# Performance work log

Measured on AMD Instinct MI355X. Metric: run time of the kernel, lower is better.

The kernel has to match this reference:

```python
import jax, jax.numpy as jnp
import numpy as np

NEG_FILL = -1.0e9
PROB_MIN = 1e-9


def _lstm_cell(x, h, c, w_ih, w_hh, b_ih, b_hh):
    # PyTorch gate order: input, forget, cell(g), output
    gates = x @ w_ih.T + h @ w_hh.T + b_ih + b_hh
    i, f, g, o = jnp.split(gates, 4, axis=-1)
    c_new = jax.nn.sigmoid(f) * c + jax.nn.sigmoid(i) * jnp.tanh(g)
    h_new = jax.nn.sigmoid(o) * jnp.tanh(c_new)
    return h_new, c_new


def setup_inputs() -> dict:
    key = jax.random.key(0)
    B, T, D, H, W = 2048, 100, 128, 256, 256
    ks = jax.random.split(key, 16)
    s_d = 1.0 / np.sqrt(D)
    s_h = 1.0 / np.sqrt(H)
    s_w = 1.0 / np.sqrt(W)
    return {
        "targets": jax.random.normal(ks[0], (B, T, D), jnp.float32),
        "h0": jax.random.normal(ks[1], (1, B, H), jnp.float32),
        "c0": jax.random.normal(ks[2], (1, B, H), jnp.float32),
        "enc_w_ih": jax.random.normal(ks[3], (4 * H, D), jnp.float32) * s_d,
        "enc_w_hh": jax.random.normal(ks[4], (4 * H, H), jnp.float32) * s_h,
        "enc_b_ih": jax.random.normal(ks[5], (4 * H,), jnp.float32) * s_h,
        "enc_b_hh": jax.random.normal(ks[6], (4 * H,), jnp.float32) * s_h,
        "dec_w_ih": jax.random.normal(ks[7], (4 * H, D), jnp.float32) * s_d,
        "dec_w_hh": jax.random.normal(ks[8], (4 * H, H), jnp.float32) * s_h,
        "dec_b_ih": jax.random.normal(ks[9], (4 * H,), jnp.float32) * s_h,
        "dec_b_hh": jax.random.normal(ks[10], (4 * H,), jnp.float32) * s_h,
        "W1": jax.random.normal(ks[11], (W, H), jnp.float32) * s_h,
        "W2": jax.random.normal(ks[12], (W, H), jnp.float32) * s_h,
        "vt": jax.random.normal(ks[13], (W,), jnp.float32) * s_w,
    }


def reference(targets, h0, c0, enc_w_ih, enc_w_hh, enc_b_ih, enc_b_hh,
              dec_w_ih, dec_w_hh, dec_b_ih, dec_b_hh, W1, W2, vt):
    B, T, D = targets.shape
    H = enc_w_hh.shape[1]

    # ---- encoder LSTM (batch_first, zero initial state) ----
    def enc_step(carry, x_t):
        h, c = carry
        h, c = _lstm_cell(x_t, h, c, enc_w_ih, enc_w_hh, enc_b_ih, enc_b_hh)
        return (h, c), h

    z = jnp.zeros((B, H), targets.dtype)
    _, enc_h = jax.lax.scan(enc_step, (z, z), jnp.swapaxes(targets, 0, 1))
    encoder_states = jnp.swapaxes(enc_h, 0, 1)  # [B, T, H]

    blend1 = encoder_states @ W1.T  # [B, T, W]

    a1 = jnp.arange(B)
    init = (h0[0], c0[0], jnp.zeros((B, T), dtype=bool), jnp.zeros_like(targets[:, 0]))

    def dec_step(carry, _):
        h, c, selected, dec_in = carry
        h, c = _lstm_cell(dec_in, h, c, dec_w_ih, dec_w_hh, dec_b_ih, dec_b_hh)
        blend2 = h @ W2.T                                   # [B, W]
        scores = jnp.tanh(blend1 + blend2[:, None, :]) @ vt  # [B, T]
        scores = jnp.where(selected, NEG_FILL, scores)
        sel = jnp.argmax(scores, axis=-1)                    # [B]
        selected = selected.at[a1, sel].set(True)
        probs = jnp.maximum(jax.nn.softmax(scores, axis=-1), PROB_MIN)
        dec_in = targets[a1, sel]                            # [B, D]
        return (h, c, selected, dec_in), probs

    _, probs = jax.lax.scan(dec_step, init, None, length=T)
    return jnp.swapaxes(probs, 0, 1)  # [B, T, T]
```

## Files before the change

### kernel.cpp

```cpp
#include <hip/hip_runtime.h>
#include <math.h>
#include <stdint.h>

#define BB   2048
#define TT   100
#define DD   128
#define HH   256
#define NEGF -1.0e9f

typedef __attribute__((ext_vector_type(8))) short short8_t;
typedef __attribute__((ext_vector_type(4))) float f32x4;

#define MFMA16(a,b,c) __builtin_amdgcn_mfma_f32_16x16x32_bf16((a),(b),(c),0,0,0)

__device__ __forceinline__ float sigmoidf_(float x){ return 1.0f/(1.0f+expf(-x)); }

__device__ __forceinline__ float tanh_fast(float x){
  x = fminf(15.f, fmaxf(-15.f, x));
  const float e = __expf(x + x);
  return (e - 1.f) * __builtin_amdgcn_rcpf(e + 1.f);
}

__device__ __forceinline__ void bf16_split3(float x, unsigned short &h,
                                            unsigned short &m, unsigned short &l){
  const unsigned u = __float_as_uint(x);
  const unsigned r = u + 0x7FFFu + ((u >> 16) & 1u);
  h = (unsigned short)(r >> 16);
  const float rem = x - __uint_as_float(r & 0xFFFF0000u);
  const unsigned u2 = __float_as_uint(rem);
  const unsigned r2 = u2 + 0x7FFFu + ((u2 >> 16) & 1u);
  m = (unsigned short)(r2 >> 16);
  const float rem2 = rem - __uint_as_float(r2 & 0xFFFF0000u);
  l = (unsigned short)(__float_as_uint(rem2) >> 16);
}

__global__ __launch_bounds__(256) void k_split3(const float* __restrict__ src,
    unsigned short* __restrict__ hi, unsigned short* __restrict__ mi,
    unsigned short* __restrict__ lo, int n){
  const int i = blockIdx.x*256 + threadIdx.x;
  if(i < n){ unsigned short h,m,l; bf16_split3(src[i], h, m, l);
             hi[i]=h; mi[i]=m; lo[i]=l; }
}

__global__ __launch_bounds__(256) void k_zero_i32(int* __restrict__ p, int n){
  int i = blockIdx.x*256 + threadIdx.x;
  if(i < n) p[i] = 0;
}

#define MFMA_X6(aH,aM,aL,bH,bM,bL,acc)            \
  do{ acc = MFMA16(aM, bM, acc);                  \
      acc = MFMA16(aH, bL, acc);                  \
      acc = MFMA16(aL, bH, acc);                  \
      acc = MFMA16(aH, bM, acc);                  \
      acc = MFMA16(aM, bH, acc);                  \
      acc = MFMA16(aH, bH, acc); }while(0)

__global__ __launch_bounds__(128) void k_gates_cell(
    const float* __restrict__ Xp, int ldx,
    const float* __restrict__ Hp,
    const unsigned short* __restrict__ WihH, const unsigned short* __restrict__ WihM,
    const unsigned short* __restrict__ WihL,
    const unsigned short* __restrict__ WhhH, const unsigned short* __restrict__ WhhM,
    const unsigned short* __restrict__ WhhL,
    const float* __restrict__ bih, const float* __restrict__ bhh,
    const float* __restrict__ Cp,
    float* __restrict__ Hout, float* __restrict__ Cout,
    float* __restrict__ Hcopy, int hstride)
{
  __shared__ alignas(16) unsigned short AsH[64*40], AsM[64*40], AsL[64*40];
  __shared__ alignas(16) unsigned short WsH[64*40], WsM[64*40], WsL[64*40];
  const int tid  = threadIdx.x;
  const int lane = tid & 63;
  const int wv   = tid >> 6;
  const int l15  = lane & 15;
  const int l4   = lane >> 4;
  const int j0   = blockIdx.x * 16;
  const int m0   = blockIdx.y * 64;

  f32x4 acc[2][4];
  #pragma unroll
  for(int a=0;a<2;a++)
    #pragma unroll
    for(int s=0;s<4;s++)
      #pragma unroll
      for(int e=0;e<4;e++) acc[a][s][e] = 0.f;

  for(int phase=0; phase<2; phase++){
    const float* Am; int lda;
    const unsigned short *WH, *WM, *WL; int ldw, nt;
    if(phase==0){ if(!Xp) continue; Am=Xp; lda=ldx;
                  WH=WihH; WM=WihM; WL=WihL; ldw=DD; nt=4; }
    else        { if(!Hp) continue; Am=Hp; lda=HH;
                  WH=WhhH; WM=WhhM; WL=WhhL; ldw=HH; nt=8; }
    for(int kt=0; kt<nt; kt++){
      const int k0 = kt*32;
      __syncthreads();
      #pragma unroll
      for(int it=0; it<4; it++){
        const int q  = it*128 + tid;
        const int r  = q >> 3;
        const int kq = (q & 7) << 2;
        const float4 v = *(const float4*)(Am + (size_t)(m0+r)*lda + k0 + kq);
        unsigned short h0,m0_,l0,h1,m1_,l1,h2,m2_,l2,h3,m3_,l3;
        bf16_split3(v.x,h0,m0_,l0); bf16_split3(v.y,h1,m1_,l1);
        bf16_split3(v.z,h2,m2_,l2); bf16_split3(v.w,h3,m3_,l3);
        *(ushort4*)&AsH[r*40+kq] = make_ushort4(h0,h1,h2,h3);
        *(ushort4*)&AsM[r*40+kq] = make_ushort4(m0_,m1_,m2_,m3_);
        *(ushort4*)&AsL[r*40+kq] = make_ushort4(l0,l1,l2,l3);
      }
      #pragma unroll
      for(int half=0; half<3; half++){
        const unsigned short* __restrict__ Wg = (half==0)?WH:((half==1)?WM:WL);
        unsigned short* Ws = (half==0)?WsH:((half==1)?WsM:WsL);
        #pragma unroll
        for(int it=0; it<2; it++){
          const int q  = it*128 + tid;
          const int c  = q >> 2;
          const int kq = (q & 3) << 3;
          const int n  = ((c>>4)*HH) + j0 + (c & 15);
          *(uint4*)&Ws[c*40+kq] = *(const uint4*)(Wg + (size_t)n*ldw + k0 + kq);
        }
      }
      __syncthreads();
      short8_t aH[2], aM[2], aL[2];
      #pragma unroll
      for(int fm=0; fm<2; fm++){
        const int r = wv*32 + fm*16 + l15;
        aH[fm] = *(const short8_t*)&AsH[r*40 + l4*8];
        aM[fm] = *(const short8_t*)&AsM[r*40 + l4*8];
        aL[fm] = *(const short8_t*)&AsL[r*40 + l4*8];
      }
      #pragma unroll
      for(int s=0; s<4; s++){
        const int c = s*16 + l15;
        const short8_t bH = *(const short8_t*)&WsH[c*40 + l4*8];
        const short8_t bM = *(const short8_t*)&WsM[c*40 + l4*8];
        const short8_t bL = *(const short8_t*)&WsL[c*40 + l4*8];
        #pragma unroll
        for(int fm=0; fm<2; fm++){
          MFMA_X6(aH[fm],aM[fm],aL[fm], bH,bM,bL, acc[fm][s]);
        }
      }
    }
  }

  const int j = j0 + l15;
  const float bi0 = bih[       j] + bhh[       j];
  const float bf0 = bih[  HH + j] + bhh[  HH + j];
  const float bg0 = bih[2*HH + j] + bhh[2*HH + j];
  const float bo0 = bih[3*HH + j] + bhh[3*HH + j];
  #pragma unroll
  for(int fm=0; fm<2; fm++){
    #pragma unroll
    for(int r=0; r<4; r++){
      const int m = m0 + wv*32 + fm*16 + l4*4 + r;
      const size_t idx = (size_t)m*HH + j;
      const float iv = acc[fm][0][r] + bi0;
      const float fv = acc[fm][1][r] + bf0;
      const float gv = acc[fm][2][r] + bg0;
      const float ov = acc[fm][3][r] + bo0;
      const float cp = Cp ? Cp[idx] : 0.f;
      const float cn = sigmoidf_(fv)*cp + sigmoidf_(iv)*tanhf(gv);
      const float hn = sigmoidf_(ov)*tanhf(cn);
      Cout[idx] = cn;
      Hout[idx] = hn;
      if(Hcopy) Hcopy[(size_t)m*hstride + j] = hn;
    }
  }
}

__global__ __launch_bounds__(128) void k_blend2(
    const float* __restrict__ Hin,
    const unsigned short* __restrict__ W2H, const unsigned short* __restrict__ W2M,
    const unsigned short* __restrict__ W2L,
    float* __restrict__ out)
{
  __shared__ alignas(16) unsigned short AsH[32*40], AsM[32*40], AsL[32*40];
  __shared__ alignas(16) unsigned short WsH[64*40], WsM[64*40], WsL[64*40];
  const int tid  = threadIdx.x;
  const int lane = tid & 63;
  const int wv   = tid >> 6;
  const int l15  = lane & 15;
  const int l4   = lane >> 4;
  const int n0   = blockIdx.x * 64;
  const int m0   = blockIdx.y * 32;

  f32x4 acc[4];
  #pragma unroll
  for(int s=0;s<4;s++)
    #pragma unroll
    for(int e=0;e<4;e++) acc[s][e] = 0.f;

  for(int kt=0; kt<8; kt++){
    const int k0 = kt*32;
    __syncthreads();
    #pragma unroll
    for(int it=0; it<2; it++){
      const int q  = it*128 + tid;
      const int r  = q >> 3;
      const int kq = (q & 7) << 2;
      const float4 v = *(const float4*)(Hin + (size_t)(m0+r)*HH + k0 + kq);
      unsigned short h0,m0_,l0,h1,m1_,l1,h2,m2_,l2,h3,m3_,l3;
      bf16_split3(v.x,h0,m0_,l0); bf16_split3(v.y,h1,m1_,l1);
      bf16_split3(v.z,h2,m2_,l2); bf16_split3(v.w,h3,m3_,l3);
      *(ushort4*)&AsH[r*40+kq] = make_ushort4(h0,h1,h2,h3);
      *(ushort4*)&AsM[r*40+kq] = make_ushort4(m0_,m1_,m2_,m3_);
      *(ushort4*)&AsL[r*40+kq] = make_ushort4(l0,l1,l2,l3);
    }
    #pragma unroll
    for(int half=0; half<3; half++){
      const unsigned short* __restrict__ Wg = (half==0)?W2H:((half==1)?W2M:W2L);
      unsigned short* Ws = (half==0)?WsH:((half==1)?WsM:WsL);
      #pragma unroll
      for(int it=0; it<2; it++){
        const int q  = it*128 + tid;
        const int c  = q >> 2;
        const int kq = (q & 3) << 3;
        const int n  = n0 + c;
        *(uint4*)&Ws[c*40+kq] = *(const uint4*)(Wg + (size_t)n*HH + k0 + kq);
      }
    }
    __syncthreads();
    const int r = wv*16 + l15;
    const short8_t aH = *(const short8_t*)&AsH[r*40 + l4*8];
    const short8_t aM = *(const short8_t*)&AsM[r*40 + l4*8];
    const short8_t aL = *(const short8_t*)&AsL[r*40 + l4*8];
    #pragma unroll
    for(int s=0; s<4; s++){
      const int c = s*16 + l15;
      const short8_t bH = *(const short8_t*)&WsH[c*40 + l4*8];
      const short8_t bM = *(const short8_t*)&WsM[c*40 + l4*8];
      const short8_t bL = *(const short8_t*)&WsL[c*40 + l4*8];
      MFMA_X6(aH,aM,aL, bH,bM,bL, acc[s]);
    }
  }
  #pragma unroll
  for(int s=0; s<4; s++)
    #pragma unroll
    for(int r=0; r<4; r++)
      out[(size_t)(m0 + wv*16 + l4*4 + r)*HH + n0 + s*16 + l15] = acc[s][r];
}

__global__ __launch_bounds__(128) void k_blend1(
    float* __restrict__ blend1,
    const unsigned short* __restrict__ W1H, const unsigned short* __restrict__ W1M,
    const unsigned short* __restrict__ W1L)
{
  __shared__ alignas(16) unsigned short AsH[32*264], AsM[32*264], AsL[32*264];
  const int tid  = threadIdx.x;
  const int lane = tid & 63;
  const int wv   = tid >> 6;
  const int l15  = lane & 15;
  const int l4   = lane >> 4;
  const size_t r0 = (size_t)blockIdx.x * 32;

  #pragma unroll
  for(int it=0; it<16; it++){
    const int q  = it*128 + tid;
    const int r  = q >> 6;
    const int kq = (q & 63) << 2;
    const float4 v = *(const float4*)(blend1 + (r0+r)*256 + kq);
    unsigned short h0,m0_,l0,h1,m1_,l1,h2,m2_,l2,h3,m3_,l3;
    bf16_split3(v.x,h0,m0_,l0); bf16_split3(v.y,h1,m1_,l1);
    bf16_split3(v.z,h2,m2_,l2); bf16_split3(v.w,h3,m3_,l3);
    *(ushort4*)&AsH[r*264+kq] = make_ushort4(h0,h1,h2,h3);
    *(ushort4*)&AsM[r*264+kq] = make_ushort4(m0_,m1_,m2_,m3_);
    *(ushort4*)&AsL[r*264+kq] = make_ushort4(l0,l1,l2,l3);
  }
  __syncthreads();

  f32x4 acc[16];
  #pragma unroll
  for(int s=0;s<16;s++)
    #pragma unroll
    for(int e=0;e<4;e++) acc[s][e] = 0.f;

  const int rb = wv*16;
  for(int kt=0; kt<8; kt++){
    const int k0 = kt*32;
    const short8_t aH = *(const short8_t*)&AsH[(rb+l15)*264 + k0 + l4*8];
    const short8_t aM = *(const short8_t*)&AsM[(rb+l15)*264 + k0 + l4*8];
    const short8_t aL = *(const short8_t*)&AsL[(rb+l15)*264 + k0 + l4*8];
    #pragma unroll
    for(int fn=0; fn<16; fn++){
      const int n = fn*16 + l15;
      const short8_t bH = *(const short8_t*)(W1H + (size_t)n*256 + k0 + l4*8);
      const short8_t bM = *(const short8_t*)(W1M + (size_t)n*256 + k0 + l4*8);
      const short8_t bL = *(const short8_t*)(W1L + (size_t)n*256 + k0 + l4*8);
      MFMA_X6(aH,aM,aL, bH,bM,bL, acc[fn]);
    }
  }
  #pragma unroll
  for(int fn=0; fn<16; fn++)
    #pragma unroll
    for(int r=0; r<4; r++)
      blend1[(r0 + rb + l4*4 + r)*256 + fn*16 + l15] = acc[fn][r];
}

__global__ __launch_bounds__(256) void k_scores(
    const float* __restrict__ blend1,
    const float* __restrict__ blend2,
    const float* __restrict__ vt,
    const float* __restrict__ targets,
    int*  __restrict__ selected,
    float* __restrict__ dec_in,
    float* __restrict__ out,
    int s)
{
  __shared__ float vt_s[256], b2_s[256], sc[128];
  __shared__ float M_s, S_s;
  __shared__ int sel_s;
  const int b = blockIdx.x;
  const int tid = threadIdx.x;
  const int lane = tid & 63;
  const int wave = tid >> 6;

  vt_s[tid] = vt[tid];
  b2_s[tid] = blend2[(size_t)b*256 + tid];
  __syncthreads();

  const float4 bb = *(const float4*)&b2_s[lane*4];
  const float4 vv = *(const float4*)&vt_s[lane*4];

  for(int it=0; it<25; it++){
    const int t = wave + it*4;
    const float4 x = *(const float4*)(blend1 + ((size_t)b*TT + t)*256 + lane*4);
    float p;
    p = tanh_fast(x.x + bb.x) * vv.x;
    p = fmaf(tanh_fast(x.y + bb.y), vv.y, p);
    p = fmaf(tanh_fast(x.z + bb.z), vv.z, p);
    p = fmaf(tanh_fast(x.w + bb.w), vv.w, p);
    #pragma unroll
    for(int off=32; off>=1; off>>=1) p += __shfl_xor(p, off, 64);
    if(lane == 0) sc[t] = p;
  }
  __syncthreads();

  if(wave == 0){
    float m1 = selected[(size_t)b*TT + lane] ? NEGF : sc[lane];
    sc[lane] = m1;
    float bestv = m1; int besti = lane;
    float m2 = 0.f;
    const int t2 = lane + 64;
    if(t2 < TT){
      m2 = selected[(size_t)b*TT + t2] ? NEGF : sc[t2];
      sc[t2] = m2;
      if(m2 > bestv){ bestv = m2; besti = t2; }
    }
    #pragma unroll
    for(int off=32; off>=1; off>>=1){
      const float ov = __shfl_xor(bestv, off, 64);
      const int   oi = __shfl_xor(besti, off, 64);
      if(ov > bestv || (ov == bestv && oi < besti)){ bestv = ov; besti = oi; }
    }
    float e = __expf(m1 - bestv);
    if(t2 < TT) e += __expf(m2 - bestv);
    #pragma unroll
    for(int off=32; off>=1; off>>=1) e += __shfl_xor(e, off, 64);
    if(lane == 0){
      M_s = bestv; S_s = e; sel_s = besti;
      selected[(size_t)b*TT + besti] = 1;
    }
  }
  __syncthreads();

  const int sel = sel_s;
  if(tid < TT){
    float p = __expf(sc[tid] - M_s) / S_s;
    out[(size_t)b*TT*TT + (size_t)s*TT + tid] = fmaxf(p, 1e-9f);
  }
  if(tid < DD){
    dec_in[(size_t)b*DD + tid] = targets[((size_t)b*TT + sel)*DD + tid];
  }
}

extern "C" void kernel_launch(void* const* d_in, const int* in_sizes, int n_in,
                              void* d_out, int out_size, void* d_ws, size_t ws_size,
                              hipStream_t stream)
{
  (void)in_sizes; (void)n_in; (void)out_size; (void)ws_size;
  const float* targets  = (const float*)d_in[0];
  const float* h0       = (const float*)d_in[1];
  const float* c0       = (const float*)d_in[2];
  const float* enc_w_ih = (const float*)d_in[3];
  const float* enc_w_hh = (const float*)d_in[4];
  const float* enc_b_ih = (const float*)d_in[5];
  const float* enc_b_hh = (const float*)d_in[6];
  const float* dec_w_ih = (const float*)d_in[7];
  const float* dec_w_hh = (const float*)d_in[8];
  const float* dec_b_ih = (const float*)d_in[9];
  const float* dec_b_hh = (const float*)d_in[10];
  const float* W1       = (const float*)d_in[11];
  const float* W2       = (const float*)d_in[12];
  const float* vt       = (const float*)d_in[13];
  float* out = (float*)d_out;

  float* ws      = (float*)d_ws;
  float* blend1  = ws;
  float* hA      = blend1 + (size_t)BB*TT*256;
  float* hB      = hA + (size_t)BB*HH;
  float* cA      = hB + (size_t)BB*HH;
  float* cB      = cA + (size_t)BB*HH;
  float* blend2  = cB + (size_t)BB*HH;
  float* dec_in  = blend2 + (size_t)BB*HH;
  int*   selected= (int*)(dec_in + (size_t)BB*DD);

  char* pc = (char*)(selected + (size_t)BB*TT);
  pc = (char*)(((uintptr_t)pc + 63) & ~(uintptr_t)63);
  unsigned short* q = (unsigned short*)pc;
  unsigned short* ewihH = q; q += (size_t)1024*128;
  unsigned short* ewihM = q; q += (size_t)1024*128;
  unsigned short* ewihL = q; q += (size_t)1024*128;
  unsigned short* ewhhH = q; q += (size_t)1024*256;
  unsigned short* ewhhM = q; q += (size_t)1024*256;
  unsigned short* ewhhL = q; q += (size_t)1024*256;
  unsigned short* dwihH = q; q += (size_t)1024*128;
  unsigned short* dwihM = q; q += (size_t)1024*128;
  unsigned short* dwihL = q; q += (size_t)1024*128;
  unsigned short* dwhhH = q; q += (size_t)1024*256;
  unsigned short* dwhhM = q; q += (size_t)1024*256;
  unsigned short* dwhhL = q; q += (size_t)1024*256;
  unsigned short* w1H   = q; q += (size_t)256*256;
  unsigned short* w1M   = q; q += (size_t)256*256;
  unsigned short* w1L   = q; q += (size_t)256*256;
  unsigned short* w2H   = q; q += (size_t)256*256;
  unsigned short* w2M   = q; q += (size_t)256*256;
  unsigned short* w2L   = q; q += (size_t)256*256;

  k_split3<<<(1024*128+255)/256, 256, 0, stream>>>(enc_w_ih, ewihH, ewihM, ewihL, 1024*128);
  k_split3<<<(1024*256+255)/256, 256, 0, stream>>>(enc_w_hh, ewhhH, ewhhM, ewhhL, 1024*256);
  k_split3<<<(1024*128+255)/256, 256, 0, stream>>>(dec_w_ih, dwihH, dwihM, dwihL, 1024*128);
  k_split3<<<(1024*256+255)/256, 256, 0, stream>>>(dec_w_hh, dwhhH, dwhhM, dwhhL, 1024*256);
  k_split3<<<(256*256+255)/256,  256, 0, stream>>>(W1, w1H, w1M, w1L, 256*256);
  k_split3<<<(256*256+255)/256,  256, 0, stream>>>(W2, w2H, w2M, w2L, 256*256);

  k_zero_i32<<<(BB*TT + 255)/256, 256, 0, stream>>>(selected, BB*TT);

  for(int t=0; t<TT; t++){
    const float* Hp = (t==0) ? nullptr : ((t&1) ? hA : hB);
    const float* Cp = (t==0) ? nullptr : ((t&1) ? cA : cB);
    float* Ho = (t&1) ? hB : hA;
    float* Co = (t&1) ? cB : cA;
    k_gates_cell<<<dim3(16,32), 128, 0, stream>>>(
        targets + (size_t)t*DD, TT*DD,
        Hp, ewihH, ewihM, ewihL, ewhhH, ewhhM, ewhhL, enc_b_ih, enc_b_hh, Cp,
        Ho, Co, blend1 + (size_t)t*256, TT*256);
  }

  k_blend1<<<BB*TT/32, 128, 0, stream>>>(blend1, w1H, w1M, w1L);

  for(int s=0; s<TT; s++){
    const float* Hp = (s==0) ? h0 : ((s&1) ? hA : hB);
    const float* Cp = (s==0) ? c0 : ((s&1) ? cA : cB);
    float* Ho = (s&1) ? hB : hA;
    float* Co = (s&1) ? cB : cA;
    const float* Xp = (s==0) ? nullptr : dec_in;
    k_gates_cell<<<dim3(16,32), 128, 0, stream>>>(
        Xp, DD, Hp, dwihH, dwihM, dwihL, dwhhH, dwhhM, dwhhL, dec_b_ih, dec_b_hh, Cp,
        Ho, Co, nullptr, 0);
    k_blend2<<<dim3(4,64), 128, 0, stream>>>(Ho, w2H, w2M, w2L, blend2);
    k_scores<<<BB, 256, 0, stream>>>(blend1, blend2, vt, targets, selected,
                                     dec_in, out, s);
  }
}
```

Measured before the change: 14.68 ms.

## Fuse encoder and decoder recurrences into persistent per-batch-slice kernels

Replaces the roughly 400 per-timestep launches (gates, blend2, scores) with two persistent kernels. Each kernel owns 16 batch rows across all timesteps and keeps h, c and selection state in registers and LDS. Weights are prepacked into an MFMA-fragment layout with the input and hidden parts concatenated into one K=384 GEMM, and blend2 becomes an fp32 FMA loop over a transposed W2. Only 128 blocks run, so each block streams the full packed weight set from global or L2 on every step, and occupancy is low.

Measured after the change: 15.94 ms. +8.6%, slower.

```diff
diff --git a/kernel.cpp b/kernel.cpp
--- a/kernel.cpp
+++ b/kernel.cpp
@@ -2,16 +2,30 @@
 #include <math.h>
 #include <stdint.h>
 
-#define BB   2048
-#define TT   100
-#define DD   128
-#define HH   256
+#define BB 2048
+#define TT 100
+#define DD 128
+#define HH 256
 #define NEGF -1.0e9f
+
+#define NBLK 128
+#define ROWS 16
+#define NTHR 512
+#define KTOT 384
+#define NKF  12
+#define ASTR 392
 
 typedef __attribute__((ext_vector_type(8))) short short8_t;
 typedef __attribute__((ext_vector_type(4))) float f32x4;
 
 #define MFMA16(a,b,c) __builtin_amdgcn_mfma_f32_16x16x32_bf16((a),(b),(c),0,0,0)
+#define MFMA_X6(aH,aM,aL,bH,bM,bL,acc)            \
+  do{ acc = MFMA16(aM, bM, acc);                  \
+      acc = MFMA16(aH, bL, acc);                  \
+      acc = MFMA16(aL, bH, acc);                  \
+      acc = MFMA16(aH, bM, acc);                  \
+      acc = MFMA16(aM, bH, acc);                  \
+      acc = MFMA16(aH, bH, acc); }while(0)
 
 __device__ __forceinline__ float sigmoidf_(float x){ return 1.0f/(1.0f+expf(-x)); }
 
@@ -42,203 +56,317 @@
              hi[i]=h; mi[i]=m; lo[i]=l; }
 }
 
-__global__ __launch_bounds__(256) void k_zero_i32(int* __restrict__ p, int n){
-  int i = blockIdx.x*256 + threadIdx.x;
-  if(i < n) p[i] = 0;
-}
-
-#define MFMA_X6(aH,aM,aL,bH,bM,bL,acc)            \
-  do{ acc = MFMA16(aM, bM, acc);                  \
-      acc = MFMA16(aH, bL, acc);                  \
-      acc = MFMA16(aL, bH, acc);                  \
-      acc = MFMA16(aH, bM, acc);                  \
-      acc = MFMA16(aM, bH, acc);                  \
-      acc = MFMA16(aH, bH, acc); }while(0)
-
-__global__ __launch_bounds__(128) void k_gates_cell(
-    const float* __restrict__ Xp, int ldx,
-    const float* __restrict__ Hp,
-    const unsigned short* __restrict__ WihH, const unsigned short* __restrict__ WihM,
-    const unsigned short* __restrict__ WihL,
-    const unsigned short* __restrict__ WhhH, const unsigned short* __restrict__ WhhM,
-    const unsigned short* __restrict__ WhhL,
+__global__ __launch_bounds__(256) void k_transpose256(const float* __restrict__ in,
+                                                      float* __restrict__ outp){
+  const int k = blockIdx.x;
+  const int n = threadIdx.x;
+  outp[k*256 + n] = in[n*256 + k];
+}
+
+__global__ __launch_bounds__(256) void k_packW(
+    const float* __restrict__ w_ih, const float* __restrict__ w_hh,
+    unsigned short* __restrict__ WfH, unsigned short* __restrict__ WfM,
+    unsigned short* __restrict__ WfL)
+{
+  const int i = blockIdx.x*256 + threadIdx.x;
+  if(i >= 1024*KTOT) return;
+  const int f    = i / (NKF*64*8);
+  const int r1   = i % (NKF*64*8);
+  const int kf   = r1 >> 9;
+  const int r2   = r1 & 511;
+  const int lane = r2 >> 3;
+  const int e    = r2 & 7;
+  const int n = f*16 + (lane & 15);
+  const int k = kf*32 + (lane >> 4)*8 + e;
+  const float w = (k < DD) ? w_ih[(size_t)n*DD + k] : w_hh[(size_t)n*HH + (k-DD)];
+  unsigned short h,m,l; bf16_split3(w,h,m,l);
+  WfH[i]=h; WfM[i]=m; WfL[i]=l;
+}
+
+__device__ __forceinline__ int swA(int row, int byteoff){
+  return row*ASTR + (((byteoff) ^ ((row & 7) << 4)) >> 1);
+}
+
+__global__ __launch_bounds__(NTHR) void k_encoder(
+    const float* __restrict__ targets,
+    const unsigned short* __restrict__ WfH, const unsigned short* __restrict__ WfM,
+    const unsigned short* __restrict__ WfL,
     const float* __restrict__ bih, const float* __restrict__ bhh,
-    const float* __restrict__ Cp,
-    float* __restrict__ Hout, float* __restrict__ Cout,
-    float* __restrict__ Hcopy, int hstride)
+    float* __restrict__ blend1)
 {
-  __shared__ alignas(16) unsigned short AsH[64*40], AsM[64*40], AsL[64*40];
-  __shared__ alignas(16) unsigned short WsH[64*40], WsM[64*40], WsL[64*40];
-  const int tid  = threadIdx.x;
+  __shared__ unsigned short AsH[ROWS*ASTR], AsM[ROWS*ASTR], AsL[ROWS*ASTR];
+  const int tid = threadIdx.x;
   const int lane = tid & 63;
-  const int wv   = tid >> 6;
-  const int l15  = lane & 15;
-  const int l4   = lane >> 4;
-  const int j0   = blockIdx.x * 16;
-  const int m0   = blockIdx.y * 64;
-
-  f32x4 acc[2][4];
+  const int wv = tid >> 6;
+  const int l15 = lane & 15, l4 = lane >> 4;
+  const int b0 = blockIdx.x * ROWS;
+
+  float bias[8];
+  #pragma unroll
+  for(int g=0; g<4; g++)
+    #pragma unroll
+    for(int c16=0; c16<2; c16++){
+      const int n = g*256 + wv*32 + c16*16 + l15;
+      bias[g*2+c16] = bih[n] + bhh[n];
+    }
+  float cst[2][4];
   #pragma unroll
   for(int a=0;a<2;a++)
     #pragma unroll
-    for(int s=0;s<4;s++)
-      #pragma unroll
-      for(int e=0;e<4;e++) acc[a][s][e] = 0.f;
-
-  for(int phase=0; phase<2; phase++){
-    const float* Am; int lda;
-    const unsigned short *WH, *WM, *WL; int ldw, nt;
-    if(phase==0){ if(!Xp) continue; Am=Xp; lda=ldx;
-                  WH=WihH; WM=WihM; WL=WihL; ldw=DD; nt=4; }
-    else        { if(!Hp) continue; Am=Hp; lda=HH;
-                  WH=WhhH; WM=WhhM; WL=WhhL; ldw=HH; nt=8; }
-    for(int kt=0; kt<nt; kt++){
-      const int k0 = kt*32;
-      __syncthreads();
-      #pragma unroll
-      for(int it=0; it<4; it++){
-        const int q  = it*128 + tid;
-        const int r  = q >> 3;
-        const int kq = (q & 7) << 2;
-        const float4 v = *(const float4*)(Am + (size_t)(m0+r)*lda + k0 + kq);
-        unsigned short h0,m0_,l0,h1,m1_,l1,h2,m2_,l2,h3,m3_,l3;
-        bf16_split3(v.x,h0,m0_,l0); bf16_split3(v.y,h1,m1_,l1);
-        bf16_split3(v.z,h2,m2_,l2); bf16_split3(v.w,h3,m3_,l3);
-        *(ushort4*)&AsH[r*40+kq] = make_ushort4(h0,h1,h2,h3);
-        *(ushort4*)&AsM[r*40+kq] = make_ushort4(m0_,m1_,m2_,m3_);
-        *(ushort4*)&AsL[r*40+kq] = make_ushort4(l0,l1,l2,l3);
-      }
-      #pragma unroll
-      for(int half=0; half<3; half++){
-        const unsigned short* __restrict__ Wg = (half==0)?WH:((half==1)?WM:WL);
-        unsigned short* Ws = (half==0)?WsH:((half==1)?WsM:WsL);
-        #pragma unroll
-        for(int it=0; it<2; it++){
-          const int q  = it*128 + tid;
-          const int c  = q >> 2;
-          const int kq = (q & 3) << 3;
-          const int n  = ((c>>4)*HH) + j0 + (c & 15);
-          *(uint4*)&Ws[c*40+kq] = *(const uint4*)(Wg + (size_t)n*ldw + k0 + kq);
-        }
-      }
-      __syncthreads();
-      short8_t aH[2], aM[2], aL[2];
-      #pragma unroll
-      for(int fm=0; fm<2; fm++){
-        const int r = wv*32 + fm*16 + l15;
-        aH[fm] = *(const short8_t*)&AsH[r*40 + l4*8];
-        aM[fm] = *(const short8_t*)&AsM[r*40 + l4*8];
-        aL[fm] = *(const short8_t*)&AsL[r*40 + l4*8];
-      }
-      #pragma unroll
-      for(int s=0; s<4; s++){
-        const int c = s*16 + l15;
-        const short8_t bH = *(const short8_t*)&WsH[c*40 + l4*8];
-        const short8_t bM = *(const short8_t*)&WsM[c*40 + l4*8];
-        const short8_t bL = *(const short8_t*)&WsL[c*40 + l4*8];
-        #pragma unroll
-        for(int fm=0; fm<2; fm++){
-          MFMA_X6(aH[fm],aM[fm],aL[fm], bH,bM,bL, acc[fm][s]);
-        }
-      }
-    }
-  }
-
-  const int j = j0 + l15;
-  const float bi0 = bih[       j] + bhh[       j];
-  const float bf0 = bih[  HH + j] + bhh[  HH + j];
-  const float bg0 = bih[2*HH + j] + bhh[2*HH + j];
-  const float bo0 = bih[3*HH + j] + bhh[3*HH + j];
-  #pragma unroll
-  for(int fm=0; fm<2; fm++){
-    #pragma unroll
-    for(int r=0; r<4; r++){
-      const int m = m0 + wv*32 + fm*16 + l4*4 + r;
-      const size_t idx = (size_t)m*HH + j;
-      const float iv = acc[fm][0][r] + bi0;
-      const float fv = acc[fm][1][r] + bf0;
-      const float gv = acc[fm][2][r] + bg0;
-      const float ov = acc[fm][3][r] + bo0;
-      const float cp = Cp ? Cp[idx] : 0.f;
-      const float cn = sigmoidf_(fv)*cp + sigmoidf_(iv)*tanhf(gv);
-      const float hn = sigmoidf_(ov)*tanhf(cn);
-      Cout[idx] = cn;
-      Hout[idx] = hn;
-      if(Hcopy) Hcopy[(size_t)m*hstride + j] = hn;
-    }
-  }
-}
-
-__global__ __launch_bounds__(128) void k_blend2(
-    const float* __restrict__ Hin,
-    const unsigned short* __restrict__ W2H, const unsigned short* __restrict__ W2M,
-    const unsigned short* __restrict__ W2L,
-    float* __restrict__ out)
-{
-  __shared__ alignas(16) unsigned short AsH[32*40], AsM[32*40], AsL[32*40];
-  __shared__ alignas(16) unsigned short WsH[64*40], WsM[64*40], WsL[64*40];
-  const int tid  = threadIdx.x;
-  const int lane = tid & 63;
-  const int wv   = tid >> 6;
-  const int l15  = lane & 15;
-  const int l4   = lane >> 4;
-  const int n0   = blockIdx.x * 64;
-  const int m0   = blockIdx.y * 32;
-
-  f32x4 acc[4];
-  #pragma unroll
-  for(int s=0;s<4;s++)
-    #pragma unroll
-    for(int e=0;e<4;e++) acc[s][e] = 0.f;
-
-  for(int kt=0; kt<8; kt++){
-    const int k0 = kt*32;
-    __syncthreads();
-    #pragma unroll
-    for(int it=0; it<2; it++){
-      const int q  = it*128 + tid;
-      const int r  = q >> 3;
-      const int kq = (q & 7) << 2;
-      const float4 v = *(const float4*)(Hin + (size_t)(m0+r)*HH + k0 + kq);
+    for(int r=0;r<4;r++) cst[a][r] = 0.f;
+
+  for(int i=tid; i<ROWS*ASTR; i+=NTHR){ AsH[i]=0; AsM[i]=0; AsL[i]=0; }
+
+  const int srow = tid >> 5;
+  const int k4   = (tid & 31) * 4;
+  const int sidx = swA(srow, k4*2);
+
+  for(int t=0; t<TT; t++){
+    __syncthreads();
+    {
+      const float4 v = *(const float4*)(targets + ((size_t)(b0+srow)*TT + t)*DD + k4);
       unsigned short h0,m0_,l0,h1,m1_,l1,h2,m2_,l2,h3,m3_,l3;
       bf16_split3(v.x,h0,m0_,l0); bf16_split3(v.y,h1,m1_,l1);
       bf16_split3(v.z,h2,m2_,l2); bf16_split3(v.w,h3,m3_,l3);
-      *(ushort4*)&AsH[r*40+kq] = make_ushort4(h0,h1,h2,h3);
-      *(ushort4*)&AsM[r*40+kq] = make_ushort4(m0_,m1_,m2_,m3_);
-      *(ushort4*)&AsL[r*40+kq] = make_ushort4(l0,l1,l2,l3);
-    }
-    #pragma unroll
-    for(int half=0; half<3; half++){
-      const unsigned short* __restrict__ Wg = (half==0)?W2H:((half==1)?W2M:W2L);
-      unsigned short* Ws = (half==0)?WsH:((half==1)?WsM:WsL);
-      #pragma unroll
-      for(int it=0; it<2; it++){
-        const int q  = it*128 + tid;
-        const int c  = q >> 2;
-        const int kq = (q & 3) << 3;
-        const int n  = n0 + c;
-        *(uint4*)&Ws[c*40+kq] = *(const uint4*)(Wg + (size_t)n*HH + k0 + kq);
-      }
-    }
-    __syncthreads();
-    const int r = wv*16 + l15;
-    const short8_t aH = *(const short8_t*)&AsH[r*40 + l4*8];
-    const short8_t aM = *(const short8_t*)&AsM[r*40 + l4*8];
-    const short8_t aL = *(const short8_t*)&AsL[r*40 + l4*8];
-    #pragma unroll
-    for(int s=0; s<4; s++){
-      const int c = s*16 + l15;
-      const short8_t bH = *(const short8_t*)&WsH[c*40 + l4*8];
-      const short8_t bM = *(const short8_t*)&WsM[c*40 + l4*8];
-      const short8_t bL = *(const short8_t*)&WsL[c*40 + l4*8];
-      MFMA_X6(aH,aM,aL, bH,bM,bL, acc[s]);
+      *(ushort4*)&AsH[sidx] = make_ushort4(h0,h1,h2,h3);
+      *(ushort4*)&AsM[sidx] = make_ushort4(m0_,m1_,m2_,m3_);
+      *(ushort4*)&AsL[sidx] = make_ushort4(l0,l1,l2,l3);
+    }
+    __syncthreads();
+    f32x4 acc[8];
+    #pragma unroll
+    for(int ff=0; ff<8; ff++){
+      acc[ff][0]=bias[ff]; acc[ff][1]=bias[ff]; acc[ff][2]=bias[ff]; acc[ff][3]=bias[ff];
+    }
+    for(int kf=0; kf<NKF; kf++){
+      const int ao = swA(l15, kf*64 + l4*16);
+      const short8_t aH = *(const short8_t*)&AsH[ao];
+      const short8_t aM = *(const short8_t*)&AsM[ao];
+      const short8_t aL = *(const short8_t*)&AsL[ao];
+      #pragma unroll
+      for(int g=0; g<4; g++)
+        #pragma unroll
+        for(int c16=0; c16<2; c16++){
+          const int f = g*16 + wv*2 + c16;
+          const size_t wo = ((size_t)(f*NKF + kf)*64 + lane)*8;
+          const short8_t bH = *(const short8_t*)(WfH + wo);
+          const short8_t bM = *(const short8_t*)(WfM + wo);
+          const short8_t bL = *(const short8_t*)(WfL + wo);
+          MFMA_X6(aH,aM,aL,bH,bM,bL, acc[g*2+c16]);
+        }
+    }
+    __syncthreads();
+    #pragma unroll
+    for(int c16=0; c16<2; c16++){
+      const int j = wv*32 + c16*16 + l15;
+      #pragma unroll
+      for(int r=0; r<4; r++){
+        const int row = l4*4 + r;
+        const float iv = acc[0+c16][r];
+        const float fv = acc[2+c16][r];
+        const float gv = acc[4+c16][r];
+        const float ov = acc[6+c16][r];
+        const float cn = sigmoidf_(fv)*cst[c16][r] + sigmoidf_(iv)*tanhf(gv);
+        const float hn = sigmoidf_(ov)*tanhf(cn);
+        cst[c16][r] = cn;
+        unsigned short sh, sm_, sl;
+        bf16_split3(hn, sh, sm_, sl);
+        const int hi = swA(row, (128 + j)*2);
+        AsH[hi] = sh; AsM[hi] = sm_; AsL[hi] = sl;
+        blend1[((size_t)(b0+row)*TT + t)*256 + j] = hn;
+      }
     }
   }
-  #pragma unroll
-  for(int s=0; s<4; s++)
+}
+
+__global__ __launch_bounds__(NTHR) void k_decoder(
+    const float* __restrict__ targets,
+    const unsigned short* __restrict__ WfH, const unsigned short* __restrict__ WfM,
+    const unsigned short* __restrict__ WfL,
+    const float* __restrict__ bih, const float* __restrict__ bhh,
+    const float* __restrict__ h0, const float* __restrict__ c0,
+    const float* __restrict__ W2t, const float* __restrict__ vt,
+    const float* __restrict__ blend1,
+    float* __restrict__ outp)
+{
+  __shared__ unsigned short AsH[ROWS*ASTR], AsM[ROWS*ASTR], AsL[ROWS*ASTR];
+  __shared__ float hs[ROWS*264];
+  __shared__ float b2s[ROWS*264];
+  __shared__ float sc[ROWS][104];
+  __shared__ float vts[256];
+  __shared__ char selc[ROWS][104];
+  const int tid = threadIdx.x;
+  const int lane = tid & 63;
+  const int wv = tid >> 6;
+  const int l15 = lane & 15, l4 = lane >> 4;
+  const int b0 = blockIdx.x * ROWS;
+
+  float bias[8];
+  #pragma unroll
+  for(int g=0; g<4; g++)
+    #pragma unroll
+    for(int c16=0; c16<2; c16++){
+      const int n = g*256 + wv*32 + c16*16 + l15;
+      bias[g*2+c16] = bih[n] + bhh[n];
+    }
+
+  for(int i=tid; i<ROWS*ASTR; i+=NTHR){ AsH[i]=0; AsM[i]=0; AsL[i]=0; }
+  if(tid < 256) vts[tid] = vt[tid];
+  for(int i=tid; i<ROWS*104; i+=NTHR) (&selc[0][0])[i] = 0;
+  {
+    const int row = tid >> 5;
+    const int k8  = (tid & 31) * 8;
+    #pragma unroll
+    for(int ii=0; ii<8; ii+=4){
+      const float4 v = *(const float4*)(h0 + (size_t)(b0+row)*HH + k8 + ii);
+      unsigned short h0_,m0_,l0,h1,m1_,l1,h2,m2_,l2,h3,m3_,l3;
+      bf16_split3(v.x,h0_,m0_,l0); bf16_split3(v.y,h1,m1_,l1);
+      bf16_split3(v.z,h2,m2_,l2); bf16_split3(v.w,h3,m3_,l3);
+      const int idx = swA(row, (128 + k8 + ii)*2);
+      *(ushort4*)&AsH[idx] = make_ushort4(h0_,h1,h2,h3);
+      *(ushort4*)&AsM[idx] = make_ushort4(m0_,m1_,m2_,m3_);
+      *(ushort4*)&AsL[idx] = make_ushort4(l0,l1,l2,l3);
+    }
+  }
+  float cst[2][4];
+  #pragma unroll
+  for(int c16=0; c16<2; c16++)
     #pragma unroll
     for(int r=0; r<4; r++)
-      out[(size_t)(m0 + wv*16 + l4*4 + r)*HH + n0 + s*16 + l15] = acc[s][r];
+      cst[c16][r] = c0[(size_t)(b0 + l4*4 + r)*HH + wv*32 + c16*16 + l15];
+
+  for(int st=0; st<TT; st++){
+    __syncthreads();
+    f32x4 acc[8];
+    #pragma unroll
+    for(int ff=0; ff<8; ff++){
+      acc[ff][0]=bias[ff]; acc[ff][1]=bias[ff]; acc[ff][2]=bias[ff]; acc[ff][3]=bias[ff];
+    }
+    for(int kf=0; kf<NKF; kf++){
+      const int ao = swA(l15, kf*64 + l4*16);
+      const short8_t aH = *(const short8_t*)&AsH[ao];
+      const short8_t aM = *(const short8_t*)&AsM[ao];
+      const short8_t aL = *(const short8_t*)&AsL[ao];
+      #pragma unroll
+      for(int g=0; g<4; g++)
+        #pragma unroll
+        for(int c16=0; c16<2; c16++){
+          const int f = g*16 + wv*2 + c16;
+          const size_t wo = ((size_t)(f*NKF + kf)*64 + lane)*8;
+          const short8_t bH = *(const short8_t*)(WfH + wo);
+          const short8_t bM = *(const short8_t*)(WfM + wo);
+          const short8_t bL = *(const short8_t*)(WfL + wo);
+          MFMA_X6(aH,aM,aL,bH,bM,bL, acc[g*2+c16]);
+        }
+    }
+    __syncthreads();
+    #pragma unroll
+    for(int c16=0; c16<2; c16++){
+      const int j = wv*32 + c16*16 + l15;
+      #pragma unroll
+      for(int r=0; r<4; r++){
+        const int row = l4*4 + r;
+        const float iv = acc[0+c16][r];
+        const float fv = acc[2+c16][r];
+        const float gv = acc[4+c16][r];
+        const float ov = acc[6+c16][r];
+        const float cn = sigmoidf_(fv)*cst[c16][r] + sigmoidf_(iv)*tanhf(gv);
+        const float hn = sigmoidf_(ov)*tanhf(cn);
+        cst[c16][r] = cn;
+        unsigned short sh, sm_, sl;
+        bf16_split3(hn, sh, sm_, sl);
+        const int hi = swA(row, (128 + j)*2);
+        AsH[hi] = sh; AsM[hi] = sm_; AsL[hi] = sl;
+        hs[row*264 + j] = hn;
+      }
+    }
+    __syncthreads();
+    {
+      const int row = tid >> 5;
+      const int n8  = (tid & 31) * 8;
+      float a8[8];
+      #pragma unroll
+      for(int i=0;i<8;i++) a8[i] = 0.f;
+      #pragma unroll 4
+      for(int k=0; k<HH; k++){
+        const float hv = hs[row*264 + k];
+        const float4 w0 = *(const float4*)(W2t + (size_t)k*HH + n8);
+        const float4 w1 = *(const float4*)(W2t + (size_t)k*HH + n8 + 4);
+        a8[0]=fmaf(hv,w0.x,a8[0]); a8[1]=fmaf(hv,w0.y,a8[1]);
+        a8[2]=fmaf(hv,w0.z,a8[2]); a8[3]=fmaf(hv,w0.w,a8[3]);
+        a8[4]=fmaf(hv,w1.x,a8[4]); a8[5]=fmaf(hv,w1.y,a8[5]);
+        a8[6]=fmaf(hv,w1.z,a8[6]); a8[7]=fmaf(hv,w1.w,a8[7]);
+      }
+      #pragma unroll
+      for(int i=0;i<8;i++) b2s[row*264 + n8 + i] = a8[i];
+    }
+    __syncthreads();
+    {
+      const int g4 = lane >> 4, l16 = lane & 15;
+      #pragma unroll
+      for(int rr=0; rr<2; rr++){
+        const int row = wv*2 + rr;
+        const float* bl  = blend1 + ((size_t)(b0+row)*TT)*256;
+        const float* b2p = &b2s[row*264];
+        for(int tb=0; tb<25; tb++){
+          const int t = tb*4 + g4;
+          float p = 0.f;
+          #pragma unroll
+          for(int q=0; q<4; q++){
+            const int k = l16*16 + q*4;
+            const float4 x   = *(const float4*)(bl + (size_t)t*256 + k);
+            const float4 b2v = *(const float4*)(b2p + k);
+            const float4 vv4 = *(const float4*)(&vts[k]);
+            p = fmaf(tanh_fast(x.x + b2v.x), vv4.x, p);
+            p = fmaf(tanh_fast(x.y + b2v.y), vv4.y, p);
+            p = fmaf(tanh_fast(x.z + b2v.z), vv4.z, p);
+            p = fmaf(tanh_fast(x.w + b2v.w), vv4.w, p);
+          }
+          #pragma unroll
+          for(int off=8; off>=1; off>>=1) p += __shfl_xor(p, off, 64);
+          if(l16 == 0) sc[row][t] = p;
+        }
+      }
+    }
+    __syncthreads();
+    #pragma unroll
+    for(int rr=0; rr<2; rr++){
+      const int row  = wv*2 + rr;
+      const int brow = b0 + row;
+      const float m1 = selc[row][lane] ? NEGF : sc[row][lane];
+      float bestv = m1; int besti = lane;
+      const int t2 = lane + 64;
+      float m2 = NEGF;
+      if(t2 < TT){
+        m2 = selc[row][t2] ? NEGF : sc[row][t2];
+        if(m2 > bestv){ bestv = m2; besti = t2; }
+      }
+      #pragma unroll
+      for(int off=32; off>=1; off>>=1){
+        const float ov = __shfl_xor(bestv, off, 64);
+        const int   oi = __shfl_xor(besti, off, 64);
+        if(ov > bestv || (ov == bestv && oi < besti)){ bestv = ov; besti = oi; }
+      }
+      float e = __expf(m1 - bestv);
+      if(t2 < TT) e += __expf(m2 - bestv);
+      #pragma unroll
+      for(int off=32; off>=1; off>>=1) e += __shfl_xor(e, off, 64);
+
+      float* orow = outp + (size_t)brow*(TT*TT) + (size_t)st*TT;
+      orow[lane] = fmaxf(__expf(m1 - bestv)/e, 1e-9f);
+      if(t2 < TT) orow[t2] = fmaxf(__expf(m2 - bestv)/e, 1e-9f);
+      if(lane == 0) selc[row][besti] = 1;
+      #pragma unroll
+      for(int dd=0; dd<2; dd++){
+        const int d = lane + dd*64;
+        const float xv = targets[((size_t)brow*TT + besti)*DD + d];
+        unsigned short th, tm, tl;
+        bf16_split3(xv, th, tm, tl);
+        const int idx = swA(row, d*2);
+        AsH[idx] = th; AsM[idx] = tm; AsL[idx] = tl;
+      }
+    }
+  }
 }
 
 __global__ __launch_bounds__(128) void k_blend1(
@@ -295,83 +423,6 @@
     #pragma unroll
     for(int r=0; r<4; r++)
       blend1[(r0 + rb + l4*4 + r)*256 + fn*16 + l15] = acc[fn][r];
-}
-
-__global__ __launch_bounds__(256) void k_scores(
-    const float* __restrict__ blend1,
-    const float* __restrict__ blend2,
-    const float* __restrict__ vt,
-    const float* __restrict__ targets,
-    int*  __restrict__ selected,
-    float* __restrict__ dec_in,
-    float* __restrict__ out,
-    int s)
-{
-  __shared__ float vt_s[256], b2_s[256], sc[128];
-  __shared__ float M_s, S_s;
-  __shared__ int sel_s;
-  const int b = blockIdx.x;
-  const int tid = threadIdx.x;
-  const int lane = tid & 63;
-  const int wave = tid >> 6;
-
-  vt_s[tid] = vt[tid];
-  b2_s[tid] = blend2[(size_t)b*256 + tid];
-  __syncthreads();
-
-  const float4 bb = *(const float4*)&b2_s[lane*4];
-  const float4 vv = *(const float4*)&vt_s[lane*4];
-
-  for(int it=0; it<25; it++){
-    const int t = wave + it*4;
-    const float4 x = *(const float4*)(blend1 + ((size_t)b*TT + t)*256 + lane*4);
-    float p;
-    p = tanh_fast(x.x + bb.x) * vv.x;
-    p = fmaf(tanh_fast(x.y + bb.y), vv.y, p);
-    p = fmaf(tanh_fast(x.z + bb.z), vv.z, p);
-    p = fmaf(tanh_fast(x.w + bb.w), vv.w, p);
-    #pragma unroll
-    for(int off=32; off>=1; off>>=1) p += __shfl_xor(p, off, 64);
-    if(lane == 0) sc[t] = p;
-  }
-  __syncthreads();
-
-  if(wave == 0){
-    float m1 = selected[(size_t)b*TT + lane] ? NEGF : sc[lane];
-    sc[lane] = m1;
-    float bestv = m1; int besti = lane;
-    float m2 = 0.f;
-    const int t2 = lane + 64;
-    if(t2 < TT){
-      m2 = selected[(size_t)b*TT + t2] ? NEGF : sc[t2];
-      sc[t2] = m2;
-      if(m2 > bestv){ bestv = m2; besti = t2; }
-    }
-    #pragma unroll
-    for(int off=32; off>=1; off>>=1){
-      const float ov = __shfl_xor(bestv, off, 64);
-      const int   oi = __shfl_xor(besti, off, 64);
-      if(ov > bestv || (ov == bestv && oi < besti)){ bestv = ov; besti = oi; }
-    }
-    float e = __expf(m1 - bestv);
-    if(t2 < TT) e += __expf(m2 - bestv);
-    #pragma unroll
-    for(int off=32; off>=1; off>>=1) e += __shfl_xor(e, off, 64);
-    if(lane == 0){
-      M_s = bestv; S_s = e; sel_s = besti;
-      selected[(size_t)b*TT + besti] = 1;
-    }
-  }
-  __syncthreads();
-
-  const int sel = sel_s;
-  if(tid < TT){
-    float p = __expf(sc[tid] - M_s) / S_s;
-    out[(size_t)b*TT*TT + (size_t)s*TT + tid] = fmaxf(p, 1e-9f);
-  }
-  if(tid < DD){
-    dec_in[(size_t)b*DD + tid] = targets[((size_t)b*TT + sel)*DD + tid];
-  }
 }
 
 extern "C" void kernel_launch(void* const* d_in, const int* in_sizes, int n_in,
@@ -393,73 +444,37 @@
   const float* W1       = (const float*)d_in[11];
   const float* W2       = (const float*)d_in[12];
   const float* vt       = (const float*)d_in[13];
-  float* out = (float*)d_out;
+  float* outp = (float*)d_out;
 
   float* ws      = (float*)d_ws;
   float* blend1  = ws;
-  float* hA      = blend1 + (size_t)BB*TT*256;
-  float* hB      = hA + (size_t)BB*HH;
-  float* cA      = hB + (size_t)BB*HH;
-  float* cB      = cA + (size_t)BB*HH;
-  float* blend2  = cB + (size_t)BB*HH;
-  float* dec_in  = blend2 + (size_t)BB*HH;
-  int*   selected= (int*)(dec_in + (size_t)BB*DD);
-
-  char* pc = (char*)(selected + (size_t)BB*TT);
+  float* W2t     = blend1 + (size_t)BB*TT*256;
+  char* pc = (char*)(W2t + 256*256);
   pc = (char*)(((uintptr_t)pc + 63) & ~(uintptr_t)63);
   unsigned short* q = (unsigned short*)pc;
-  unsigned short* ewihH = q; q += (size_t)1024*128;
-  unsigned short* ewihM = q; q += (size_t)1024*128;
-  unsigned short* ewihL = q; q += (size_t)1024*128;
-  unsigned short* ewhhH = q; q += (size_t)1024*256;
-  unsigned short* ewhhM = q; q += (size_t)1024*256;
-  unsigned short* ewhhL = q; q += (size_t)1024*256;
-  unsigned short* dwihH = q; q += (size_t)1024*128;
-  unsigned short* dwihM = q; q += (size_t)1024*128;
-  unsigned short* dwihL = q; q += (size_t)1024*128;
-  unsigned short* dwhhH = q; q += (size_t)1024*256;
-  unsigned short* dwhhM = q; q += (size_t)1024*256;
-  unsigned short* dwhhL = q; q += (size_t)1024*256;
-  unsigned short* w1H   = q; q += (size_t)256*256;
-  unsigned short* w1M   = q; q += (size_t)256*256;
-  unsigned short* w1L   = q; q += (size_t)256*256;
-  unsigned short* w2H   = q; q += (size_t)256*256;
-  unsigned short* w2M   = q; q += (size_t)256*256;
-  unsigned short* w2L   = q; q += (size_t)256*256;
-
-  k_split3<<<(1024*128+255)/256, 256, 0, stream>>>(enc_w_ih, ewihH, ewihM, ewihL, 1024*128);
-  k_split3<<<(1024*256+255)/256, 256, 0, stream>>>(enc_w_hh, ewhhH, ewhhM, ewhhL, 1024*256);
-  k_split3<<<(1024*128+255)/256, 256, 0, stream>>>(dec_w_ih, dwihH, dwihM, dwihL, 1024*128);
-  k_split3<<<(1024*256+255)/256, 256, 0, stream>>>(dec_w_hh, dwhhH, dwhhM, dwhhL, 1024*256);
-  k_split3<<<(256*256+255)/256,  256, 0, stream>>>(W1, w1H, w1M, w1L, 256*256);
-  k_split3<<<(256*256+255)/256,  256, 0, stream>>>(W2, w2H, w2M, w2L, 256*256);
-
-  k_zero_i32<<<(BB*TT + 255)/256, 256, 0, stream>>>(selected, BB*TT);
-
-  for(int t=0; t<TT; t++){
-    const float* Hp = (t==0) ? nullptr : ((t&1) ? hA : hB);
-    const float* Cp = (t==0) ? nullptr : ((t&1) ? cA : cB);
-    float* Ho = (t&1) ? hB : hA;
-    float* Co = (t&1) ? cB : cA;
-    k_gates_cell<<<dim3(16,32), 128, 0, stream>>>(
-        targets + (size_t)t*DD, TT*DD,
-        Hp, ewihH, ewihM, ewihL, ewhhH, ewhhM, ewhhL, enc_b_ih, enc_b_hh, Cp,
-        Ho, Co, blend1 + (size_t)t*256, TT*256);
-  }
+  const size_t WFSZ = (size_t)1024*KTOT;
+  unsigned short* eWfH = q; q += WFSZ;
+  unsigned short* eWfM = q; q += WFSZ;
+  unsigned short* eWfL = q; q += WFSZ;
+  unsigned short* dWfH = q; q += WFSZ;
+  unsigned short* dWfM = q; q += WFSZ;
+  unsigned short* dWfL = q; q += WFSZ;
+  unsigned short* w1H  = q; q += (size_t)256*256;
+  unsigned short* w1M  = q; q += (size_t)256*256;
+  unsigned short* w1L  = q; q += (size_t)256*256;
+
+  const int packGrid = (1024*KTOT + 255)/256;
+  k_packW<<<packGrid, 256, 0, stream>>>(enc_w_ih, enc_w_hh, eWfH, eWfM, eWfL);
+  k_packW<<<packGrid, 256, 0, stream>>>(dec_w_ih, dec_w_hh, dWfH, dWfM, dWfL);
+  k_split3<<<(256*256+255)/256, 256, 0, stream>>>(W1, w1H, w1M, w1L, 256*256);
+  k_transpose256<<<256, 256, 0, stream>>>(W2, W2t);
+
+  k_encoder<<<NBLK, NTHR, 0, stream>>>(targets, eWfH, eWfM, eWfL,
+                                       enc_b_ih, enc_b_hh, blend1);
 
   k_blend1<<<BB*TT/32, 128, 0, stream>>>(blend1, w1H, w1M, w1L);
 
-  for(int s=0; s<TT; s++){
-    const float* Hp = (s==0) ? h0 : ((s&1) ? hA : hB);
-    const float* Cp = (s==0) ? c0 : ((s&1) ? cA : cB);
-    float* Ho = (s&1) ? hB : hA;
-    float* Co = (s&1) ? cB : cA;
-    const float* Xp = (s==0) ? nullptr : dec_in;
-    k_gates_cell<<<dim3(16,32), 128, 0, stream>>>(
-        Xp, DD, Hp, dwihH, dwihM, dwihL, dwhhH, dwhhM, dwhhL, dec_b_ih, dec_b_hh, Cp,
-        Ho, Co, nullptr, 0);
-    k_blend2<<<dim3(4,64), 128, 0, stream>>>(Ho, w2H, w2M, w2L, blend2);
-    k_scores<<<BB, 256, 0, stream>>>(blend1, blend2, vt, targets, selected,
-                                     dec_in, out, s);
-  }
-}
+  k_decoder<<<NBLK, NTHR, 0, stream>>>(targets, dWfH, dWfM, dWfL,
+                                       dec_b_ih, dec_b_hh, h0, c0,
+                                       W2t, vt, blend1, outp);
+}
```
